# Kernel tuning notes

Hardware: AMD Instinct MI355X
Metric: run time of the kernel (lower is better)

## Reference

```python
import jax, jax.numpy as jnp
import numpy as np

G, N, D, L, T = 64, 64, 128, 4, 10
SLOPE = 0.01
BN_EPS = 1e-5


def _gin(x, adj, mask, W1, b1, W2, b2, eps):
    # x: [B,N,D], adj: [B,N,N], mask: [B,N] bool
    agg = jnp.einsum('bnm,bmd->bnd', adj, x)
    h = (1.0 + eps) * x + agg
    h = jax.nn.leaky_relu(h @ W1 + b1, SLOPE)
    h = h @ W2 + b2
    return h * mask[..., None].astype(h.dtype)


def _masked_bn(h, mask, gamma, beta):
    # training-mode BatchNorm1d over the masked (valid) rows only
    m = mask[..., None].astype(h.dtype)
    cnt = jnp.sum(m)
    mean = jnp.sum(h * m, axis=(0, 1)) / cnt
    var = jnp.sum(((h - mean) ** 2) * m, axis=(0, 1)) / cnt  # biased, as BN
    hn = (h - mean) * jax.lax.rsqrt(var + BN_EPS) * gamma + beta
    return jnp.where(mask[..., None], hn, h)


def _seg_mean(v, idx, num_segments):
    s = jax.ops.segment_sum(v, idx, num_segments=num_segments)
    c = jax.ops.segment_sum(jnp.ones((v.shape[0],), v.dtype), idx, num_segments=num_segments)
    return s / jnp.maximum(c, 1.0).reshape((num_segments,) + (1,) * (v.ndim - 1))


def setup_inputs() -> dict:
    key = jax.random.key(0)
    ks = jax.random.split(key, 16)
    S = G * N
    # original graphs: symmetric binary adjacency, no self loops
    a = (jax.random.uniform(ks[0], (G, N, N)) > 0.9).astype(jnp.float32)
    a = jnp.triu(a, 1)
    original_adj = a + a.transpose(0, 2, 1)
    original_mask = jnp.ones((G, N), dtype=bool)
    # node-deleted policy: subgraph s of graph s//N deletes node s%N
    graph_idx = jnp.repeat(jnp.arange(G), N)
    deleted = jnp.tile(jnp.arange(N), G)
    mask = jnp.ones((S, N), dtype=bool).at[jnp.arange(S), deleted].set(False)
    mf = mask.astype(jnp.float32)
    adj = original_adj[graph_idx] * mf[:, :, None] * mf[:, None, :]
    x = jax.random.normal(ks[1], (S, N, D), dtype=jnp.float32)
    sc = 1.0 / np.sqrt(D)
    inp = dict(
        x=x, adj=adj, original_adj=original_adj,
        gnn_W1=jax.random.normal(ks[2], (L, D, D)) * sc,
        gnn_b1=jnp.zeros((L, D)),
        gnn_W2=jax.random.normal(ks[3], (L, D, D)) * sc,
        gnn_b2=jnp.zeros((L, D)),
        gnn_eps=jnp.zeros((L,)),
        gs_W1=jax.random.normal(ks[4], (L, D, D)) * sc,
        gs_b1=jnp.zeros((L, D)),
        gs_W2=jax.random.normal(ks[5], (L, D, D)) * sc,
        gs_b2=jnp.zeros((L, D)),
        gs_eps=jnp.zeros((L,)),
        bn_gamma=jnp.ones((L, D)), bn_beta=jnp.zeros((L, D)),
        bns_gamma=jnp.ones((L, D)), bns_beta=jnp.zeros((L, D)),
        fin_W1=jax.random.normal(ks[6], (D, 2 * D)) * sc,
        fin_b1=jnp.zeros((2 * D,)),
        fin_W2=jax.random.normal(ks[7], (2 * D, T)) * (1.0 / np.sqrt(2 * D)),
        fin_b2=jnp.zeros((T,)),
        mask=mask, original_mask=original_mask, graph_idx=graph_idx,
    )
    return inp


def reference(x, adj, original_adj, gnn_W1, gnn_b1, gnn_W2, gnn_b2, gnn_eps,
              gs_W1, gs_b1, gs_W2, gs_b2, gs_eps,
              bn_gamma, bn_beta, bns_gamma, bns_beta,
              fin_W1, fin_b1, fin_W2, fin_b2,
              mask, original_mask, graph_idx):
    for i in range(L):
        h1 = _gin(x, adj, mask, gnn_W1[i], gnn_b1[i], gnn_W2[i], gnn_b2[i], gnn_eps[i])
        h1 = _masked_bn(h1, mask, bn_gamma[i], bn_beta[i])
        x_sum = _seg_mean(x, graph_idx, G)  # [G,N,D] scatter-mean over subgraphs
        h2 = _gin(x_sum, original_adj, original_mask, gs_W1[i], gs_b1[i], gs_W2[i], gs_b2[i], gs_eps[i])
        h2 = _masked_bn(h2, original_mask, bns_gamma[i], bns_beta[i])
        x = jax.nn.leaky_relu(h1 + h2[graph_idx], SLOPE)
    num_nodes = jnp.sum(mask, axis=-1).astype(x.dtype)  # [S]
    h_sub = jnp.sum(x, axis=1) / num_nodes[:, None]     # mean pool per subgraph
    h_graph = _seg_mean(h_sub, graph_idx, G)            # [G,D]
    out = jax.nn.leaky_relu(h_graph @ fin_W1 + fin_b1, SLOPE) @ fin_W2 + fin_b2
    return out
```

## Files before the change

### kernel.cpp

```cpp
#include <hip/hip_runtime.h>
#include <hip/hip_bf16.h>


typedef __bf16 bf16x8 __attribute__((ext_vector_type(8)));
typedef float f32x4 __attribute__((ext_vector_type(4)));
typedef unsigned short us8 __attribute__((ext_vector_type(8)));
typedef unsigned short us4 __attribute__((ext_vector_type(4)));
typedef unsigned u32x4 __attribute__((ext_vector_type(4)));
typedef unsigned u32x2 __attribute__((ext_vector_type(2)));

__device__ __forceinline__ unsigned short f2b(float f) {
  unsigned u = __builtin_bit_cast(unsigned, f);
  u += 0x7FFFu + ((u >> 16) & 1u);
  return (unsigned short)(u >> 16);
}
__device__ __forceinline__ unsigned cvtpk(float lo, float hi) {
  unsigned r;
  asm("v_cvt_pk_bf16_f32 %0, %1, %2" : "=v"(r) : "v"(lo), "v"(hi));
  return r;
}
__device__ __forceinline__ float b2f(unsigned short h) {
  return __builtin_bit_cast(float, (unsigned)h << 16);
}
__device__ __forceinline__ f32x4 mm(bf16x8 a, bf16x8 b, f32x4 c) {
  return __builtin_amdgcn_mfma_f32_16x16x32_bf16(a, b, c, 0, 0, 0);
}
__device__ __forceinline__ bf16x8 frag(const char* base, int row, int Kelems, int k0) {
  int off = (row * Kelems + k0) * 2;
  off ^= (row & 7) << 4;
  return *(const bf16x8*)(base + off);
}
__device__ __forceinline__ float lk(float v) { return fmaxf(v, 0.01f * v); }

__global__ __launch_bounds__(256) void k_prep(const float* __restrict__ g1,
    const float* __restrict__ g2, const float* __restrict__ s1,
    const float* __restrict__ s2, unsigned short* __restrict__ wt) {
  int b = blockIdx.x;
  int l = b >> 2, j = b & 3;
  const float* src = (j == 0 ? g1 : j == 1 ? g2 : j == 2 ? s1 : s2) + l * 16384;
  unsigned short* dst = wt + b * 16384;
  for (int e = threadIdx.x; e < 16384; e += 256) {
    int n = e >> 7, k = e & 127;
    dst[e] = f2b(src[k * 128 + n]);
  }
}

__global__ __launch_bounds__(256) void k_pack(const float* __restrict__ src,
                                              unsigned short* __restrict__ dst) {
  int sub = blockIdx.x, t = threadIdx.x;
  const float* p = src + (size_t)sub * 4096 + (t >> 2) * 64 + (t & 3) * 16;
  unsigned bits = 0;
  #pragma unroll
  for (int j4 = 0; j4 < 4; ++j4) {
    float4 v = *(const float4*)(p + j4 * 4);
    bits |= (unsigned)(v.x != 0.f) << (j4 * 4);
    bits |= (unsigned)(v.y != 0.f) << (j4 * 4 + 1);
    bits |= (unsigned)(v.z != 0.f) << (j4 * 4 + 2);
    bits |= (unsigned)(v.w != 0.f) << (j4 * 4 + 3);
  }
  dst[(size_t)sub * 256 + t] = (unsigned short)bits;
}

__global__ __launch_bounds__(256) void k_castseg(const float* __restrict__ x,
    unsigned short* __restrict__ xw, float* __restrict__ pxs) {
  int b2 = blockIdx.x, bb = b2 >> 2, c = b2 & 3, t = threadIdx.x;
  int e0 = c * 2048 + t * 8;
  float acc[8];
  #pragma unroll
  for (int j = 0; j < 8; ++j) acc[j] = 0.f;
  for (int ss = 0; ss < 16; ++ss) {
    size_t sb = ((size_t)bb * 16 + ss) * 8192 + e0;
    float4 v0 = *(const float4*)(x + sb);
    float4 v1 = *(const float4*)(x + sb + 4);
    acc[0] += v0.x; acc[1] += v0.y; acc[2] += v0.z; acc[3] += v0.w;
    acc[4] += v1.x; acc[5] += v1.y; acc[6] += v1.z; acc[7] += v1.w;
    u32x4 pk;
    pk.x = cvtpk(v0.x, v0.y); pk.y = cvtpk(v0.z, v0.w);
    pk.z = cvtpk(v1.x, v1.y); pk.w = cvtpk(v1.z, v1.w);
    *(us8*)(xw + sb) = __builtin_bit_cast(us8, pk);
  }
  float* o = pxs + (size_t)bb * 8192 + e0;
  *(float4*)o = make_float4(acc[0], acc[1], acc[2], acc[3]);
  *(float4*)(o + 4) = make_float4(acc[4], acc[5], acc[6], acc[7]);
}

template<int LAST>
__global__ __launch_bounds__(256) void k_xpart(const unsigned short* __restrict__ h1T,
    const unsigned short* __restrict__ h2T, const float* __restrict__ bnA,
    const float* __restrict__ bnB, const float* __restrict__ bnsA,
    const float* __restrict__ bnsB, float* __restrict__ pxsT,
    float* __restrict__ ppool) {
  int b2 = blockIdx.x, bb = b2 >> 2, c = b2 & 3, g = bb >> 2;
  int t = threadIdx.x;
  int d = c * 32 + (t >> 3), n0 = (t & 7) * 8;
  size_t off = (size_t)d * 64 + n0;
  float A1 = bnA[d], B1 = bnB[d];
  float A2 = bnsA[d], B2 = bnsB[d];
  float hb[8];
  {
    us8 v = *(const us8*)(h2T + (size_t)g * 8192 + off);
    #pragma unroll
    for (int j = 0; j < 8; ++j) hb[j] = fmaf(b2f(v[j]), A2, B2);
  }
  float acc[8];
  #pragma unroll
  for (int j = 0; j < 8; ++j) acc[j] = 0.f;
  for (int ss = 0; ss < 16; ++ss) {
    int s = bb * 16 + ss;
    int del = s & 63;
    us8 a = *(const us8*)(h1T + (size_t)s * 8192 + off);
    #pragma unroll
    for (int j = 0; j < 8; ++j) {
      float hv = ((n0 + j) != del) ? fmaf(b2f(a[j]), A1, B1) : 0.f;
      acc[j] += lk(hv + hb[j]);
    }
  }
  if (!LAST) {
    float* o = pxsT + (size_t)bb * 8192 + off;
    *(float4*)o       = make_float4(acc[0], acc[1], acc[2], acc[3]);
    *(float4*)(o + 4) = make_float4(acc[4], acc[5], acc[6], acc[7]);
  } else {
    float s8 = ((acc[0] + acc[1]) + (acc[2] + acc[3])) + ((acc[4] + acc[5]) + (acc[6] + acc[7]));
    s8 += __shfl_xor(s8, 1, 64);
    s8 += __shfl_xor(s8, 2, 64);
    s8 += __shfl_xor(s8, 4, 64);
    if ((t & 7) == 0) ppool[(size_t)bb * 128 + d] = s8;
  }
}

template<int FIRST>
__global__ __launch_bounds__(512, 4) void k_gin(
    const unsigned short* __restrict__ xw, unsigned short* __restrict__ h1T,
    const unsigned short* __restrict__ h2prev, unsigned short* __restrict__ h2out,
    const float* __restrict__ pxs,
    const unsigned short* __restrict__ badj, const unsigned short* __restrict__ boadj,
    const unsigned short* __restrict__ W1g, const unsigned short* __restrict__ W2g,
    const unsigned short* __restrict__ W1s, const unsigned short* __restrict__ W2s,
    const float* __restrict__ b1g, const float* __restrict__ b2g,
    const float* __restrict__ b1s, const float* __restrict__ b2s,
    const float* __restrict__ epg, const float* __restrict__ epss,
    const float* __restrict__ bnA, const float* __restrict__ bnB,
    const float* __restrict__ bnsA, const float* __restrict__ bnsB,
    float* __restrict__ p1s, float* __restrict__ p1q,
    float* __restrict__ p2s, float* __restrict__ p2q) {
  __shared__ __align__(16) char lds[40960];
  char* ldsAdj = lds;
  char* ldsB   = lds + 8192;
  char* ldsC   = lds + 24576;

  const int tid = threadIdx.x;
  const int bid = blockIdx.x;
  const bool SUB = bid < 4096;
  const int lb = SUB ? bid : bid - 4096;
  const int wv = tid >> 6, ln = tid & 63;
  const int lr = ln & 15, lkh = ln >> 4;
  const int wrow = wv * 16 + lr;
  const float ep1 = 1.0f + (SUB ? epg[0] : epss[0]);
  const int del = SUB ? (bid & 63) : -1;
  const unsigned short* W1t = SUB ? W1g : W1s;
  const unsigned short* W2t = SUB ? W2g : W2s;

  bf16x8 w1f[4], w2f[4];
  #pragma unroll
  for (int kk = 0; kk < 4; ++kk) {
    w1f[kk] = *(const bf16x8*)(W1t + (size_t)wrow * 128 + kk * 32 + lkh * 8);
    w2f[kk] = *(const bf16x8*)(W2t + (size_t)wrow * 128 + kk * 32 + lkh * 8);
  }
  const float bb1 = (SUB ? b1g : b1s)[wrow];
  const float bb2 = (SUB ? b2g : b2s)[wrow];

  {
    const unsigned char* bits =
        (const unsigned char*)(SUB ? badj + (size_t)lb * 256 : boadj + (size_t)lb * 256);
    unsigned char bbt = bits[tid];
    int row = tid >> 3, o = tid & 7;
    unsigned short ep1b = f2b(ep1);
    us8 v;
    #pragma unroll
    for (int j = 0; j < 8; ++j) v[j] = ((bbt >> j) & 1) ? (unsigned short)0x3F80 : (unsigned short)0;
    int j0 = row - o * 8;
    if (j0 >= 0 && j0 < 8) v[j0] = ep1b;
    int e = tid * 8;
    *(us8*)(ldsAdj + ((e << 1) ^ ((row & 7) << 4))) = v;
  }
  if (FIRST) {
    if (SUB) {
      const unsigned short* xg = xw + (size_t)bid * 8192;
      for (int e = tid * 8; e < 8192; e += 4096)
        *(us8*)(ldsC + e * 2) = *(const us8*)(xg + e);
    } else {
      const float* p = pxs + (size_t)lb * 4 * 8192;
      int e0 = tid * 16;
      #pragma unroll
      for (int cc = 0; cc < 4; ++cc) {
        float4 s = {0.f, 0.f, 0.f, 0.f};
        #pragma unroll
        for (int qt = 0; qt < 4; ++qt) {
          float4 v = *(const float4*)(p + qt * 8192 + e0 + cc * 4);
          s.x += v.x; s.y += v.y; s.z += v.z; s.w += v.w;
        }
        u32x2 pk;
        pk.x = cvtpk(s.x * 0.015625f, s.y * 0.015625f);
        pk.y = cvtpk(s.z * 0.015625f, s.w * 0.015625f);
        *(us4*)(ldsC + (e0 + cc * 4) * 2) = __builtin_bit_cast(us4, pk);
      }
    }
    __syncthreads();
    int d = tid & 127, mg = (tid >> 7) * 16;
    #pragma unroll
    for (int mb = 0; mb < 16; mb += 8) {
      us8 v;
      #pragma unroll
      for (int j = 0; j < 8; ++j)
        v[j] = *(const unsigned short*)(ldsC + ((mg + mb + j) << 8) + (d << 1));
      *(us8*)(ldsB + (((d << 7) + ((mg + mb) << 1)) ^ ((d & 7) << 4))) = v;
    }
  } else {
    int d = tid >> 2, n0 = (tid & 3) * 16;
    if (SUB) {
      const unsigned short* h1g = h1T + (size_t)bid * 8192 + d * 64 + n0;
      const unsigned short* h2g = h2prev + (size_t)(bid >> 6) * 8192 + d * 64 + n0;
      float A1 = bnA[d], B1 = bnB[d];
      float A2 = bnsA[d], B2 = bnsB[d];
      #pragma unroll
      for (int cc = 0; cc < 2; ++cc) {
        us8 a = *(const us8*)(h1g + cc * 8);
        us8 b = *(const us8*)(h2g + cc * 8);
        float xv[8];
        #pragma unroll
        for (int j = 0; j < 8; ++j) {
          int m = n0 + cc * 8 + j;
          float hv = (m != del) ? fmaf(b2f(a[j]), A1, B1) : 0.f;
          xv[j] = lk(hv + fmaf(b2f(b[j]), A2, B2));
        }
        u32x4 pk;
        pk.x = cvtpk(xv[0], xv[1]); pk.y = cvtpk(xv[2], xv[3]);
        pk.z = cvtpk(xv[4], xv[5]); pk.w = cvtpk(xv[6], xv[7]);
        *(us8*)(ldsB + (((d * 64 + n0 + cc * 8) * 2) ^ ((d & 7) << 4))) = __builtin_bit_cast(us8, pk);
      }
    } else {
      const float* p = pxs + (size_t)lb * 4 * 8192 + d * 64 + n0;
      #pragma unroll
      for (int cc = 0; cc < 4; ++cc) {
        float4 s = {0.f, 0.f, 0.f, 0.f};
        #pragma unroll
        for (int qt = 0; qt < 4; ++qt) {
          float4 v = *(const float4*)(p + qt * 8192 + cc * 4);
          s.x += v.x; s.y += v.y; s.z += v.z; s.w += v.w;
        }
        u32x2 pk;
        pk.x = cvtpk(s.x * 0.015625f, s.y * 0.015625f);
        pk.y = cvtpk(s.z * 0.015625f, s.w * 0.015625f);
        *(us4*)(ldsB + (((d * 64 + n0 + cc * 4) * 2) ^ ((d & 7) << 4))) = __builtin_bit_cast(us4, pk);
      }
    }
  }
  __syncthreads();

  {
    f32x4 acc[4] = {};
    #pragma unroll
    for (int rt = 0; rt < 4; ++rt) {
      #pragma unroll
      for (int k0 = 0; k0 < 64; k0 += 32) {
        bf16x8 a = frag(ldsAdj, rt * 16 + lr, 64, k0 + lkh * 8);
        bf16x8 b = frag(ldsB, wrow, 64, k0 + lkh * 8);
        acc[rt] = mm(a, b, acc[rt]);
      }
    }
    #pragma unroll
    for (int rt = 0; rt < 4; ++rt) {
      unsigned p01 = cvtpk(acc[rt][0], acc[rt][1]);
      unsigned p23 = cvtpk(acc[rt][2], acc[rt][3]);
      int r0 = rt * 16 + lkh * 4;
      *(unsigned short*)(ldsC + ((((r0 + 0) << 8) + (wrow << 1)) ^ (((r0 + 0) & 7) << 4))) = (unsigned short)p01;
      *(unsigned short*)(ldsC + ((((r0 + 1) << 8) + (wrow << 1)) ^ (((r0 + 1) & 7) << 4))) = (unsigned short)(p01 >> 16);
      *(unsigned short*)(ldsC + ((((r0 + 2) << 8) + (wrow << 1)) ^ (((r0 + 2) & 7) << 4))) = (unsigned short)p23;
      *(unsigned short*)(ldsC + ((((r0 + 3) << 8) + (wrow << 1)) ^ (((r0 + 3) & 7) << 4))) = (unsigned short)(p23 >> 16);
    }
  }
  __syncthreads();

  #pragma unroll
  for (int rt = 0; rt < 4; ++rt) {
    f32x4 acc = {};
    #pragma unroll
    for (int kk = 0; kk < 4; ++kk) {
      bf16x8 a = frag(ldsC, rt * 16 + lr, 128, kk * 32 + lkh * 8);
      acc = mm(a, w1f[kk], acc);
    }
    float u0 = lk(acc[0] + bb1), u1 = lk(acc[1] + bb1);
    float u2 = lk(acc[2] + bb1), u3 = lk(acc[3] + bb1);
    unsigned p01 = cvtpk(u0, u1);
    unsigned p23 = cvtpk(u2, u3);
    int r0 = rt * 16 + lkh * 4;
    *(unsigned short*)(ldsB + ((((r0 + 0) << 8) + (wrow << 1)) ^ (((r0 + 0) & 7) << 4))) = (unsigned short)p01;
    *(unsigned short*)(ldsB + ((((r0 + 1) << 8) + (wrow << 1)) ^ (((r0 + 1) & 7) << 4))) = (unsigned short)(p01 >> 16);
    *(unsigned short*)(ldsB + ((((r0 + 2) << 8) + (wrow << 1)) ^ (((r0 + 2) & 7) << 4))) = (unsigned short)p23;
    *(unsigned short*)(ldsB + ((((r0 + 3) << 8) + (wrow << 1)) ^ (((r0 + 3) & 7) << 4))) = (unsigned short)(p23 >> 16);
  }
  __syncthreads();

  {
    float sm = 0.f, sq = 0.f;
    #pragma unroll
    for (int rt = 0; rt < 4; ++rt) {
      f32x4 acc = {};
      #pragma unroll
      for (int kk = 0; kk < 4; ++kk) {
        bf16x8 a = frag(ldsB, rt * 16 + lr, 128, kk * 32 + lkh * 8);
        acc = mm(a, w2f[kk], acc);
      }
      float v0 = acc[0] + bb2, v1 = acc[1] + bb2, v2 = acc[2] + bb2, v3 = acc[3] + bb2;
      int m0 = rt * 16 + lkh * 4;
      if (m0 + 0 == del) v0 = 0.f;
      if (m0 + 1 == del) v1 = 0.f;
      if (m0 + 2 == del) v2 = 0.f;
      if (m0 + 3 == del) v3 = 0.f;
      sm += v0 + v1 + v2 + v3;
      sq += v0 * v0 + v1 * v1 + v2 * v2 + v3 * v3;
      u32x2 pk;
      pk.x = cvtpk(v0, v1);
      pk.y = cvtpk(v2, v3);
      *(us4*)(ldsC + (((wrow * 64 + m0) * 2) ^ ((wrow & 7) << 4))) = __builtin_bit_cast(us4, pk);
    }
    sm += __shfl_xor(sm, 16, 64); sm += __shfl_xor(sm, 32, 64);
    sq += __shfl_xor(sq, 16, 64); sq += __shfl_xor(sq, 32, 64);
    if (ln < 16) {
      float* ps = SUB ? p1s + (size_t)bid * 128 : p2s + (size_t)lb * 128;
      float* pq = SUB ? p1q + (size_t)bid * 128 : p2q + (size_t)lb * 128;
      ps[wrow] = sm;
      pq[wrow] = sq;
    }
  }
  __syncthreads();

  unsigned short* hout = SUB ? h1T + (size_t)bid * 8192 : h2out + (size_t)lb * 8192;
  {
    int e0 = tid * 16;
    int d = e0 >> 6;
    *(us8*)(hout + e0)     = *(const us8*)(ldsC + (((e0)     * 2) ^ ((d & 7) << 4)));
    *(us8*)(hout + e0 + 8) = *(const us8*)(ldsC + (((e0 + 8) * 2) ^ ((d & 7) << 4)));
  }
}

__global__ __launch_bounds__(256) void k_bnred(const float* __restrict__ p1s,
    const float* __restrict__ p1q, float* __restrict__ q1s, float* __restrict__ q1q) {
  __shared__ float red[512];
  int b = blockIdx.x, tid = threadIdx.x;
  int d = tid & 127, jh = tid >> 7;
  float s = 0.f, q = 0.f;
  for (int j = b * 64 + jh; j < b * 64 + 64; j += 2) {
    s += p1s[(size_t)j * 128 + d];
    q += p1q[(size_t)j * 128 + d];
  }
  red[tid] = s; red[256 + tid] = q;
  __syncthreads();
  if (tid < 128) {
    q1s[(size_t)b * 128 + d] = red[d] + red[d + 128];
    q1q[(size_t)b * 128 + d] = red[256 + d] + red[384 + d];
  }
}

__global__ __launch_bounds__(128) void k_bnfin(const float* __restrict__ q1s,
    const float* __restrict__ q1q, const float* __restrict__ p2s,
    const float* __restrict__ p2q, const float* __restrict__ gam1,
    const float* __restrict__ bet1, const float* __restrict__ gam2,
    const float* __restrict__ bet2, float* __restrict__ bnA, float* __restrict__ bnB,
    float* __restrict__ bnsA, float* __restrict__ bnsB) {
  int d = threadIdx.x;
  float s = 0.f, q = 0.f, s2 = 0.f, q2 = 0.f;
  for (int j = 0; j < 64; ++j) {
    s  += q1s[j * 128 + d];  q  += q1q[j * 128 + d];
    s2 += p2s[j * 128 + d];  q2 += p2q[j * 128 + d];
  }
  const float cnt1 = 4096.0f * 63.0f;
  float mean = s / cnt1;
  float var = q / cnt1 - mean * mean;
  float A = gam1[d] * rsqrtf(var + 1e-5f);
  bnA[d] = A; bnB[d] = bet1[d] - mean * A;
  float mean2 = s2 / 4096.0f;
  float var2 = q2 / 4096.0f - mean2 * mean2;
  float A2 = gam2[d] * rsqrtf(var2 + 1e-5f);
  bnsA[d] = A2; bnsB[d] = bet2[d] - mean2 * A2;
}

__global__ __launch_bounds__(256) void k_final(const float* __restrict__ ppool,
    const float* __restrict__ W1, const float* __restrict__ b1,
    const float* __restrict__ W2, const float* __restrict__ b2,
    float* __restrict__ out) {
  __shared__ float hg[128];
  __shared__ float z[256];
  int g = blockIdx.x, t = threadIdx.x;
  if (t < 128) {
    float s = ppool[(size_t)(g * 4 + 0) * 128 + t] + ppool[(size_t)(g * 4 + 1) * 128 + t]
            + ppool[(size_t)(g * 4 + 2) * 128 + t] + ppool[(size_t)(g * 4 + 3) * 128 + t];
    hg[t] = s * (1.0f / (63.0f * 64.0f));
  }
  __syncthreads();
  float a = b1[t];
  for (int d = 0; d < 128; ++d) a = fmaf(hg[d], W1[d * 256 + t], a);
  z[t] = lk(a);
  __syncthreads();
  if (t < 10) {
    float o = b2[t];
    for (int j = 0; j < 256; ++j) o = fmaf(z[j], W2[j * 10 + t], o);
    out[g * 10 + t] = o;
  }
}

extern "C" void kernel_launch(void* const* d_in, const int* in_sizes, int n_in,
                              void* d_out, int out_size, void* d_ws, size_t ws_size,
                              hipStream_t stream) {
  (void)in_sizes; (void)n_in; (void)out_size; (void)ws_size;
  const float* x    = (const float*)d_in[0];
  const float* adj  = (const float*)d_in[1];
  const float* oadj = (const float*)d_in[2];
  const float* gW1  = (const float*)d_in[3];
  const float* gb1  = (const float*)d_in[4];
  const float* gW2  = (const float*)d_in[5];
  const float* gb2  = (const float*)d_in[6];
  const float* geps = (const float*)d_in[7];
  const float* sW1  = (const float*)d_in[8];
  const float* sb1  = (const float*)d_in[9];
  const float* sW2  = (const float*)d_in[10];
  const float* sb2  = (const float*)d_in[11];
  const float* seps = (const float*)d_in[12];
  const float* bng  = (const float*)d_in[13];
  const float* bnb  = (const float*)d_in[14];
  const float* bnsg = (const float*)d_in[15];
  const float* bnsb = (const float*)d_in[16];
  const float* fW1  = (const float*)d_in[17];
  const float* fb1  = (const float*)d_in[18];
  const float* fW2  = (const float*)d_in[19];
  const float* fb2  = (const float*)d_in[20];
  float* out = (float*)d_out;

  char* w = (char*)d_ws;
  unsigned short* xw   = (unsigned short*)w; w += 67108864;
  unsigned short* h1T  = (unsigned short*)w; w += 67108864;
  unsigned short* h2a  = (unsigned short*)w; w += 1048576;
  unsigned short* h2b  = (unsigned short*)w; w += 1048576;
  unsigned short* badj = (unsigned short*)w; w += 2097152;
  unsigned short* boadj= (unsigned short*)w; w += 32768;
  unsigned short* wt   = (unsigned short*)w; w += 524288;
  float* pxs  = (float*)w;          w += 8388608;
  float* p1s  = (float*)w;          w += 2097152;
  float* p1q  = (float*)w;          w += 2097152;
  float* p2s  = (float*)w;          w += 32768;
  float* p2q  = (float*)w;          w += 32768;
  float* q1s  = (float*)w;          w += 32768;
  float* q1q  = (float*)w;          w += 32768;
  float* bnA  = (float*)w;          w += 512;
  float* bnB  = (float*)w;          w += 512;
  float* bnsA = (float*)w;          w += 512;
  float* bnsB = (float*)w;          w += 512;
  float* ppool= (float*)w;          w += 131072;

  unsigned short* h2buf[2] = {h2a, h2b};

  k_prep<<<16, 256, 0, stream>>>(gW1, gW2, sW1, sW2, wt);
  k_pack<<<4096, 256, 0, stream>>>(adj, badj);
  k_pack<<<64, 256, 0, stream>>>(oadj, boadj);
  k_castseg<<<1024, 256, 0, stream>>>(x, xw, pxs);

  for (int i = 0; i < 4; ++i) {
    unsigned short* h2prev = h2buf[(i + 1) & 1];
    unsigned short* h2cur  = h2buf[i & 1];
    if (i > 0)
      k_xpart<0><<<1024, 256, 0, stream>>>(h1T, h2prev, bnA, bnB, bnsA, bnsB, pxs, ppool);
    if (i == 0)
      k_gin<1><<<4160, 512, 0, stream>>>(xw, h1T, h2prev, h2cur, pxs, badj, boadj,
          wt + 0 * 16384, wt + 1 * 16384, wt + 2 * 16384, wt + 3 * 16384,
          gb1, gb2, sb1, sb2, geps, seps, bnA, bnB, bnsA, bnsB, p1s, p1q, p2s, p2q);
    else
      k_gin<0><<<4160, 512, 0, stream>>>(xw, h1T, h2prev, h2cur, pxs, badj, boadj,
          wt + (i * 4 + 0) * 16384, wt + (i * 4 + 1) * 16384,
          wt + (i * 4 + 2) * 16384, wt + (i * 4 + 3) * 16384,
          gb1 + i * 128, gb2 + i * 128, sb1 + i * 128, sb2 + i * 128,
          geps + i, seps + i, bnA, bnB, bnsA, bnsB, p1s, p1q, p2s, p2q);
    k_bnred<<<64, 256, 0, stream>>>(p1s, p1q, q1s, q1q);
    k_bnfin<<<1, 128, 0, stream>>>(q1s, q1q, p2s, p2q, bng + i * 128,
        bnb + i * 128, bnsg + i * 128, bnsb + i * 128, bnA, bnB, bnsA, bnsB);
  }
  k_xpart<1><<<1024, 256, 0, stream>>>(h1T, h2buf[1], bnA, bnB, bnsA, bnsB, pxs, ppool);
  k_final<<<64, 256, 0, stream>>>(ppool, fW1, fb1, fW2, fb2, out);
}
```

Measured before the change: 422.4 us.

## Hoist global loads before LDS adjacency build, write GIN output directly, merge pack launches

The global loads of x and h1/h2 tiles are now issued before the adjacency bitmask is expanded into LDS, so their latency overlaps that ALU work. The final output is stored straight to global memory from MFMA registers, which removes the LDS staging pass and one block barrier. The two adjacency pack launches are merged into one grid. In exchange, the direct stores are small 8-byte writes that may coalesce less well than the earlier 16-byte row copies.

```diff
diff --git a/kernel.cpp b/kernel.cpp
--- a/kernel.cpp
+++ b/kernel.cpp
@@ -45,9 +45,14 @@
   }
 }
 
-__global__ __launch_bounds__(256) void k_pack(const float* __restrict__ src,
-                                              unsigned short* __restrict__ dst) {
-  int sub = blockIdx.x, t = threadIdx.x;
+__global__ __launch_bounds__(256) void k_pack(const float* __restrict__ adj,
+    const float* __restrict__ oadj, unsigned short* __restrict__ badj,
+    unsigned short* __restrict__ boadj) {
+  int bid = blockIdx.x, t = threadIdx.x;
+  bool SUB = bid < 4096;
+  int sub = SUB ? bid : bid - 4096;
+  const float* src = SUB ? adj : oadj;
+  unsigned short* dst = SUB ? badj : boadj;
   const float* p = src + (size_t)sub * 4096 + (t >> 2) * 64 + (t & 3) * 16;
   unsigned bits = 0;
   #pragma unroll
@@ -169,26 +174,38 @@
   const float bb1 = (SUB ? b1g : b1s)[wrow];
   const float bb2 = (SUB ? b2g : b2s)[wrow];
 
-  {
-    const unsigned char* bits =
-        (const unsigned char*)(SUB ? badj + (size_t)lb * 256 : boadj + (size_t)lb * 256);
-    unsigned char bbt = bits[tid];
-    int row = tid >> 3, o = tid & 7;
-    unsigned short ep1b = f2b(ep1);
-    us8 v;
-    #pragma unroll
-    for (int j = 0; j < 8; ++j) v[j] = ((bbt >> j) & 1) ? (unsigned short)0x3F80 : (unsigned short)0;
-    int j0 = row - o * 8;
-    if (j0 >= 0 && j0 < 8) v[j0] = ep1b;
-    int e = tid * 8;
-    *(us8*)(ldsAdj + ((e << 1) ^ ((row & 7) << 4))) = v;
-  }
+  const unsigned char* bits =
+      (const unsigned char*)(SUB ? badj + (size_t)lb * 256 : boadj + (size_t)lb * 256);
+  unsigned char bbt = bits[tid];
+
   if (FIRST) {
     if (SUB) {
       const unsigned short* xg = xw + (size_t)bid * 8192;
-      for (int e = tid * 8; e < 8192; e += 4096)
-        *(us8*)(ldsC + e * 2) = *(const us8*)(xg + e);
+      us8 x0 = *(const us8*)(xg + tid * 8);
+      us8 x1 = *(const us8*)(xg + tid * 8 + 4096);
+      {
+        int row = tid >> 3, o = tid & 7;
+        unsigned short ep1b = f2b(ep1);
+        us8 v;
+        #pragma unroll
+        for (int j = 0; j < 8; ++j) v[j] = ((bbt >> j) & 1) ? (unsigned short)0x3F80 : (unsigned short)0;
+        int j0 = row - o * 8;
+        if (j0 >= 0 && j0 < 8) v[j0] = ep1b;
+        *(us8*)(ldsAdj + ((tid * 16) ^ ((row & 7) << 4))) = v;
+      }
+      *(us8*)(ldsC + tid * 16) = x0;
+      *(us8*)(ldsC + tid * 16 + 8192) = x1;
     } else {
+      {
+        int row = tid >> 3, o = tid & 7;
+        unsigned short ep1b = f2b(ep1);
+        us8 v;
+        #pragma unroll
+        for (int j = 0; j < 8; ++j) v[j] = ((bbt >> j) & 1) ? (unsigned short)0x3F80 : (unsigned short)0;
+        int j0 = row - o * 8;
+        if (j0 >= 0 && j0 < 8) v[j0] = ep1b;
+        *(us8*)(ldsAdj + ((tid * 16) ^ ((row & 7) << 4))) = v;
+      }
       const float* p = pxs + (size_t)lb * 4 * 8192;
       int e0 = tid * 16;
       #pragma unroll
@@ -220,18 +237,31 @@
     if (SUB) {
       const unsigned short* h1g = h1T + (size_t)bid * 8192 + d * 64 + n0;
       const unsigned short* h2g = h2prev + (size_t)(bid >> 6) * 8192 + d * 64 + n0;
+      us8 a0 = *(const us8*)(h1g);
+      us8 a1 = *(const us8*)(h1g + 8);
+      us8 b0 = *(const us8*)(h2g);
+      us8 b1 = *(const us8*)(h2g + 8);
+      {
+        int row = tid >> 3, o = tid & 7;
+        unsigned short ep1b = f2b(ep1);
+        us8 v;
+        #pragma unroll
+        for (int j = 0; j < 8; ++j) v[j] = ((bbt >> j) & 1) ? (unsigned short)0x3F80 : (unsigned short)0;
+        int j0 = row - o * 8;
+        if (j0 >= 0 && j0 < 8) v[j0] = ep1b;
+        *(us8*)(ldsAdj + ((tid * 16) ^ ((row & 7) << 4))) = v;
+      }
       float A1 = bnA[d], B1 = bnB[d];
       float A2 = bnsA[d], B2 = bnsB[d];
+      us8 av[2] = {a0, a1}, bv[2] = {b0, b1};
       #pragma unroll
       for (int cc = 0; cc < 2; ++cc) {
-        us8 a = *(const us8*)(h1g + cc * 8);
-        us8 b = *(const us8*)(h2g + cc * 8);
         float xv[8];
         #pragma unroll
         for (int j = 0; j < 8; ++j) {
           int m = n0 + cc * 8 + j;
-          float hv = (m != del) ? fmaf(b2f(a[j]), A1, B1) : 0.f;
-          xv[j] = lk(hv + fmaf(b2f(b[j]), A2, B2));
+          float hv = (m != del) ? fmaf(b2f(av[cc][j]), A1, B1) : 0.f;
+          xv[j] = lk(hv + fmaf(b2f(bv[cc][j]), A2, B2));
         }
         u32x4 pk;
         pk.x = cvtpk(xv[0], xv[1]); pk.y = cvtpk(xv[2], xv[3]);
@@ -239,6 +269,16 @@
         *(us8*)(ldsB + (((d * 64 + n0 + cc * 8) * 2) ^ ((d & 7) << 4))) = __builtin_bit_cast(us8, pk);
       }
     } else {
+      {
+        int row = tid >> 3, o = tid & 7;
+        unsigned short ep1b = f2b(ep1);
+        us8 v;
+        #pragma unroll
+        for (int j = 0; j < 8; ++j) v[j] = ((bbt >> j) & 1) ? (unsigned short)0x3F80 : (unsigned short)0;
+        int j0 = row - o * 8;
+        if (j0 >= 0 && j0 < 8) v[j0] = ep1b;
+        *(us8*)(ldsAdj + ((tid * 16) ^ ((row & 7) << 4))) = v;
+      }
       const float* p = pxs + (size_t)lb * 4 * 8192 + d * 64 + n0;
       #pragma unroll
       for (int cc = 0; cc < 4; ++cc) {
@@ -302,6 +342,7 @@
   __syncthreads();
 
   {
+    unsigned short* hout = SUB ? h1T + (size_t)bid * 8192 : h2out + (size_t)lb * 8192;
     float sm = 0.f, sq = 0.f;
     #pragma unroll
     for (int rt = 0; rt < 4; ++rt) {
@@ -322,7 +363,7 @@
       u32x2 pk;
       pk.x = cvtpk(v0, v1);
       pk.y = cvtpk(v2, v3);
-      *(us4*)(ldsC + (((wrow * 64 + m0) * 2) ^ ((wrow & 7) << 4))) = __builtin_bit_cast(us4, pk);
+      *(us4*)(hout + wrow * 64 + m0) = __builtin_bit_cast(us4, pk);
     }
     sm += __shfl_xor(sm, 16, 64); sm += __shfl_xor(sm, 32, 64);
     sq += __shfl_xor(sq, 16, 64); sq += __shfl_xor(sq, 32, 64);
@@ -332,15 +373,6 @@
       ps[wrow] = sm;
       pq[wrow] = sq;
     }
-  }
-  __syncthreads();
-
-  unsigned short* hout = SUB ? h1T + (size_t)bid * 8192 : h2out + (size_t)lb * 8192;
-  {
-    int e0 = tid * 16;
-    int d = e0 >> 6;
-    *(us8*)(hout + e0)     = *(const us8*)(ldsC + (((e0)     * 2) ^ ((d & 7) << 4)));
-    *(us8*)(hout + e0 + 8) = *(const us8*)(ldsC + (((e0 + 8) * 2) ^ ((d & 7) << 4)));
   }
 }
 
@@ -460,8 +492,7 @@
   unsigned short* h2buf[2] = {h2a, h2b};
 
   k_prep<<<16, 256, 0, stream>>>(gW1, gW2, sW1, sW2, wt);
-  k_pack<<<4096, 256, 0, stream>>>(adj, badj);
-  k_pack<<<64, 256, 0, stream>>>(oadj, boadj);
+  k_pack<<<4160, 256, 0, stream>>>(adj, oadj, badj, boadj);
   k_castseg<<<1024, 256, 0, stream>>>(x, xw, pxs);
 
   for (int i = 0; i < 4; ++i) {
```

New measurement: 447.3 us. +5.9%, slower.
